# Optimization experiments

Measured on AMD Instinct MI355X. Metric: run time of the kernel, lower is better.

## Reference

```python
import jax, jax.numpy as jnp
import numpy as np

B, N, D = 16, 16384, 256
H, W = 128, 128  # N == H*W: coords cover the grid exactly once (collision-free scatter)
K = 3


def setup_inputs() -> dict:
    key = jax.random.key(0)
    k1, k2, k3, k4 = jax.random.split(key, 4)
    x = jax.random.normal(k1, (B, N, D), dtype=jnp.float32)
    # coords: per-batch random permutation of all grid cells -> unique (gx, gy) per batch
    perm = jax.vmap(lambda k: jax.random.permutation(k, H * W))(jax.random.split(k2, B))  # (B, N)
    gx = perm % W
    gy = perm // W
    coords = jnp.stack([gx, gy], axis=-1).astype(jnp.int32)  # (B, N, 2), [...,0]=x, [...,1]=y
    # depthwise Conv2d params: weight (D, 1, K, K), bias (D,)  (torch kaiming-uniform-ish scale)
    bound = 1.0 / np.sqrt(K * K)
    conv_w = jax.random.uniform(k3, (D, 1, K, K), minval=-bound, maxval=bound, dtype=jnp.float32)
    conv_b = jax.random.uniform(k4, (D,), minval=-bound, maxval=bound, dtype=jnp.float32)
    return {"x": x, "coords": coords, "conv_w": conv_w, "conv_b": conv_b}


def reference(x, coords, conv_w, conv_b):
    b, n, d = x.shape
    # normalize coords to zero-based bounding box (per batch min, as in torch)
    min_c = coords.min(axis=1, keepdims=True)
    gc = coords - min_c
    max_c = gc.max(axis=1).max(axis=0)
    Hh = int(max_c[1]) + 1
    Ww = int(max_c[0]) + 1
    if Hh * Ww > 256 * 256:
        return x  # safety guard: skip mixing
    gx = gc[..., 0]
    gy = gc[..., 1]
    flat = gy * Ww + gx  # (B, N) flattened spatial index
    x_T = jnp.swapaxes(x, 1, 2)  # (B, D, N)
    # scatter: (B, D, H*W) dense grid, one vmap'd scatter per batch element
    scatter = lambda xt, f: jnp.zeros((d, Hh * Ww), x.dtype).at[:, f].set(xt)
    grid = jax.vmap(scatter)(x_T, flat).reshape(b, d, Hh, Ww)
    # depthwise conv (groups = D) with SAME-style padding k//2, then exact (erf) GELU
    out_grid = jax.lax.conv_general_dilated(
        grid, conv_w,
        window_strides=(1, 1),
        padding=[(K // 2, K // 2), (K // 2, K // 2)],
        feature_group_count=d,
    ) + conv_b[None, :, None, None]
    out_grid = jax.nn.gelu(out_grid, approximate=False)
    # gather back at the same positions, residual add
    out_flat = out_grid.reshape(b, d, Hh * Ww)
    gathered = jax.vmap(lambda g, f: g[:, f])(out_flat, flat)  # (B, D, N)
    return x + jnp.swapaxes(gathered, 1, 2)
```

## Files before the change

kernel.cpp:

```cpp
#include <hip/hip_runtime.h>
#include <hip/hip_bf16.h>

#define BB 16
#define NN 16384
#define DD 256
#define GW 128
#define TS 16
#define HS 18

__global__ __launch_bounds__(256) void build_inv_kernel(
    const int* __restrict__ coords, int* __restrict__ inv) {
  int i = blockIdx.x * blockDim.x + threadIdx.x;
  int b = i >> 14;
  int gx = coords[2 * (size_t)i];
  int gy = coords[2 * (size_t)i + 1];
  inv[(b << 14) + (gy << 7) + gx] = i & (NN - 1);
}

__global__ __launch_bounds__(256, 4) void mixer_kernel(
    const float* __restrict__ x, const float* __restrict__ cw,
    const float* __restrict__ cb, const int* __restrict__ inv,
    float* __restrict__ out) {
  __shared__ int s_inv[HS][HS];

  const int id = blockIdx.x;
  const int rem = id >> 3;
  const int b = ((id & 7) << 1) + (rem >> 6);
  const int tile = rem & 63;
  const int gy0 = (tile >> 3) * TS;
  const int gx0 = (tile & 7) * TS;

  const int c = threadIdx.x;

  float w[9];
#pragma unroll
  for (int j = 0; j < 9; ++j) w[j] = cw[c * 9 + j];
  const float bias = cb[c];

  for (int t = c; t < HS * HS; t += 256) {
    const int wy = t / HS, wx = t % HS;
    const int gy = gy0 - 1 + wy, gx = gx0 - 1 + wx;
    int nv = -1;
    if ((unsigned)gy < (unsigned)GW && (unsigned)gx < (unsigned)GW)
      nv = inv[(b << 14) + (gy << 7) + gx];
    s_inv[wy][wx] = nv;
  }
  __syncthreads();

  const float* __restrict__ xb = x + ((size_t)b << 22);
  float* __restrict__ ob = out + ((size_t)b << 22);

  float v[4][HS];
#pragma unroll
  for (int r = 0; r < 3; ++r) {
#pragma unroll
    for (int j = 0; j < HS; ++j) {
      int ns = __builtin_amdgcn_readfirstlane(s_inv[r][j]);
      v[r][j] = (ns >= 0) ? xb[((size_t)ns << 8) + c] : 0.0f;
    }
  }

#pragma unroll
  for (int iy = 0; iy < TS; ++iy) {
    if (iy + 3 < HS) {
#pragma unroll
      for (int j = 0; j < HS; ++j) {
        int ns = __builtin_amdgcn_readfirstlane(s_inv[iy + 3][j]);
        v[(iy + 3) & 3][j] = (ns >= 0) ? xb[((size_t)ns << 8) + c] : 0.0f;
      }
    }
#pragma unroll
    for (int ix = 0; ix < TS; ++ix) {
      float a = bias;
#pragma unroll
      for (int ky = 0; ky < 3; ++ky)
#pragma unroll
        for (int kx = 0; kx < 3; ++kx)
          a = fmaf(w[ky * 3 + kx], v[(iy + ky) & 3][ix + kx], a);
      const int n = __builtin_amdgcn_readfirstlane(s_inv[iy + 1][ix + 1]);
      const float g = 0.5f * a * (1.0f + erff(a * 0.70710678118654752f));
      __builtin_nontemporal_store(v[(iy + 1) & 3][ix + 1] + g,
                                  &ob[((size_t)n << 8) + c]);
    }
  }
}

extern "C" void kernel_launch(void* const* d_in, const int* in_sizes, int n_in,
                              void* d_out, int out_size, void* d_ws,
                              size_t ws_size, hipStream_t stream) {
  const float* x = (const float*)d_in[0];
  const int* coords = (const int*)d_in[1];
  const float* cw = (const float*)d_in[2];
  const float* cb = (const float*)d_in[3];
  float* out = (float*)d_out;
  int* inv = (int*)d_ws;

  {
    dim3 grid((BB * NN) / 256), block(256);
    build_inv_kernel<<<grid, block, 0, stream>>>(coords, inv);
  }
  {
    dim3 grid(BB * (GW / TS) * (GW / TS)), block(256);
    mixer_kernel<<<grid, block, 0, stream>>>(x, cw, cb, inv, out);
  }
}
```

Measured before the change: 122.2 us.

## Vectorize channels per lane and split tile rows across waves

Each lane now handles four channels with 128-bit loads and stores, and each of the four waves in a block processes four rows of the 16x16 tile instead of one thread per channel walking all rows. Out-of-grid neighbours read from a zero row in workspace, which removes the per-load branch. The sliding window is now three columns rather than a four-row register ring, so each wave reloads its halo rows and global traffic rises from about 1.27x to roughly 3x the input. The occupancy hint in launch bounds is dropped.

New measurement: 174.8 us. 43.1% more time.

```diff
diff --git a/kernel.cpp b/kernel.cpp
--- a/kernel.cpp
+++ b/kernel.cpp
@@ -3,24 +3,40 @@
 
 #define BB 16
 #define NN 16384
-#define DD 256
 #define GW 128
 #define TS 16
 #define HS 18
 
+typedef float f32x4 __attribute__((ext_vector_type(4)));
+
 __global__ __launch_bounds__(256) void build_inv_kernel(
-    const int* __restrict__ coords, int* __restrict__ inv) {
+    const int* __restrict__ coords, int* __restrict__ inv,
+    float* __restrict__ zrow) {
   int i = blockIdx.x * blockDim.x + threadIdx.x;
   int b = i >> 14;
   int gx = coords[2 * (size_t)i];
   int gy = coords[2 * (size_t)i + 1];
   inv[(b << 14) + (gy << 7) + gx] = i & (NN - 1);
+  if (blockIdx.x == 0) zrow[threadIdx.x] = 0.0f;
 }
 
-__global__ __launch_bounds__(256, 4) void mixer_kernel(
+#define LOADCOL(iyv, j, col)                                            \
+  do {                                                                  \
+    int n0 = __builtin_amdgcn_readfirstlane(s_inv[(iyv) + 0][j]);       \
+    int n1 = __builtin_amdgcn_readfirstlane(s_inv[(iyv) + 1][j]);       \
+    int n2 = __builtin_amdgcn_readfirstlane(s_inv[(iyv) + 2][j]);       \
+    const float* p0 = (n0 >= 0) ? xb + ((size_t)n0 << 8) : zrow;        \
+    const float* p1 = (n1 >= 0) ? xb + ((size_t)n1 << 8) : zrow;        \
+    const float* p2 = (n2 >= 0) ? xb + ((size_t)n2 << 8) : zrow;        \
+    col[0] = *(const f32x4*)(p0 + c4);                                  \
+    col[1] = *(const f32x4*)(p1 + c4);                                  \
+    col[2] = *(const f32x4*)(p2 + c4);                                  \
+  } while (0)
+
+__global__ __launch_bounds__(256) void mixer_kernel(
     const float* __restrict__ x, const float* __restrict__ cw,
     const float* __restrict__ cb, const int* __restrict__ inv,
-    float* __restrict__ out) {
+    const float* __restrict__ zrow, float* __restrict__ out) {
   __shared__ int s_inv[HS][HS];
 
   const int id = blockIdx.x;
@@ -30,57 +46,62 @@
   const int gy0 = (tile >> 3) * TS;
   const int gx0 = (tile & 7) * TS;
 
-  const int c = threadIdx.x;
+  const int tid = threadIdx.x;
+  const int lane = tid & 63;
+  const int wv = tid >> 6;
+  const int c4 = lane << 2;
 
-  float w[9];
-#pragma unroll
-  for (int j = 0; j < 9; ++j) w[j] = cw[c * 9 + j];
-  const float bias = cb[c];
-
-  for (int t = c; t < HS * HS; t += 256) {
-    const int wy = t / HS, wx = t % HS;
+  for (int t = tid; t < HS * HS; t += 256) {
+    const int wy = t / HS, wx = t - wy * HS;
     const int gy = gy0 - 1 + wy, gx = gx0 - 1 + wx;
     int nv = -1;
     if ((unsigned)gy < (unsigned)GW && (unsigned)gx < (unsigned)GW)
       nv = inv[(b << 14) + (gy << 7) + gx];
     s_inv[wy][wx] = nv;
   }
+
+  f32x4 wq[9], bq;
+#pragma unroll
+  for (int cc = 0; cc < 4; ++cc) {
+    bq[cc] = cb[c4 + cc];
+#pragma unroll
+    for (int j = 0; j < 9; ++j) wq[j][cc] = cw[(c4 + cc) * 9 + j];
+  }
   __syncthreads();
 
   const float* __restrict__ xb = x + ((size_t)b << 22);
   float* __restrict__ ob = out + ((size_t)b << 22);
 
-  float v[4][HS];
 #pragma unroll
-  for (int r = 0; r < 3; ++r) {
-#pragma unroll
-    for (int j = 0; j < HS; ++j) {
-      int ns = __builtin_amdgcn_readfirstlane(s_inv[r][j]);
-      v[r][j] = (ns >= 0) ? xb[((size_t)ns << 8) + c] : 0.0f;
-    }
-  }
-
-#pragma unroll
-  for (int iy = 0; iy < TS; ++iy) {
-    if (iy + 3 < HS) {
-#pragma unroll
-      for (int j = 0; j < HS; ++j) {
-        int ns = __builtin_amdgcn_readfirstlane(s_inv[iy + 3][j]);
-        v[(iy + 3) & 3][j] = (ns >= 0) ? xb[((size_t)ns << 8) + c] : 0.0f;
-      }
-    }
+  for (int k = 0; k < 4; ++k) {
+    const int iy = (wv << 2) + k;
+    f32x4 cA[3], cB[3], cC[3];
+    LOADCOL(iy, 0, cA);
+    LOADCOL(iy, 1, cB);
 #pragma unroll
     for (int ix = 0; ix < TS; ++ix) {
-      float a = bias;
+      LOADCOL(iy, ix + 2, cC);
+      f32x4 a = bq;
+      a += wq[0] * cA[0];
+      a += wq[1] * cB[0];
+      a += wq[2] * cC[0];
+      a += wq[3] * cA[1];
+      a += wq[4] * cB[1];
+      a += wq[5] * cC[1];
+      a += wq[6] * cA[2];
+      a += wq[7] * cB[2];
+      a += wq[8] * cC[2];
+      f32x4 res;
 #pragma unroll
-      for (int ky = 0; ky < 3; ++ky)
-#pragma unroll
-        for (int kx = 0; kx < 3; ++kx)
-          a = fmaf(w[ky * 3 + kx], v[(iy + ky) & 3][ix + kx], a);
+      for (int cc = 0; cc < 4; ++cc) {
+        const float av = a[cc];
+        const float ge = 0.5f * av * (1.0f + erff(av * 0.70710678118654752f));
+        res[cc] = cB[1][cc] + ge;
+      }
       const int n = __builtin_amdgcn_readfirstlane(s_inv[iy + 1][ix + 1]);
-      const float g = 0.5f * a * (1.0f + erff(a * 0.70710678118654752f));
-      __builtin_nontemporal_store(v[(iy + 1) & 3][ix + 1] + g,
-                                  &ob[((size_t)n << 8) + c]);
+      __builtin_nontemporal_store(res, (f32x4*)(ob + ((size_t)n << 8) + c4));
+      cA[0] = cB[0]; cA[1] = cB[1]; cA[2] = cB[2];
+      cB[0] = cC[0]; cB[1] = cC[1]; cB[2] = cC[2];
     }
   }
 }
@@ -94,13 +115,14 @@
   const float* cb = (const float*)d_in[3];
   float* out = (float*)d_out;
   int* inv = (int*)d_ws;
+  float* zrow = (float*)d_ws + (size_t)BB * NN;
 
   {
     dim3 grid((BB * NN) / 256), block(256);
-    build_inv_kernel<<<grid, block, 0, stream>>>(coords, inv);
+    build_inv_kernel<<<grid, block, 0, stream>>>(coords, inv, zrow);
   }
   {
     dim3 grid(BB * (GW / TS) * (GW / TS)), block(256);
-    mixer_kernel<<<grid, block, 0, stream>>>(x, cw, cb, inv, out);
+    mixer_kernel<<<grid, block, 0, stream>>>(x, cw, cb, inv, zrow, out);
   }
 }
```
